# Optimization experiments

Hardware: AMD Instinct MI355X
Metric: run time of the kernel (lower is better)

## Reference

```python
import jax, jax.numpy as jnp
import numpy as np

V = 400000
F = 800000
J = 23
B = 16
PARENTS = np.array([-1, 0, 1, 1, 3, 4, 5, 4, 7, 4, 9, 1, 11, 12, 13, 12, 15, 12, 17, 0, 19, 0, 21])


def setup_inputs() -> dict:
    key = jax.random.key(0)
    ks = jax.random.split(key, 11)
    skin = jax.random.uniform(ks[2], (1, V, J), dtype=jnp.float32)
    skin = skin / skin.sum(-1, keepdims=True)  # convex skinning weights
    return {
        "vertices": jax.random.normal(ks[0], (1, V, 3), jnp.float32),
        "joints": jax.random.normal(ks[1], (1, J, 3), jnp.float32),
        "skinning": skin,
        "joint_0": jax.random.normal(ks[3], (1, 3), jnp.float32),
        "joint_2": jax.random.normal(ks[4], (1, 3), jnp.float32),
        "joint_3": jax.random.normal(ks[5], (1, 3), jnp.float32),
        "joint_4": jax.random.normal(ks[6], (1, 3), jnp.float32),
        "joint_5": jax.random.normal(ks[7], (1, 3), jnp.float32),
        "displacement": jax.random.normal(ks[8], (1, 1, 3), jnp.float32),
        "random_dis": jax.random.normal(ks[9], (3,), jnp.float32),
        "faces": jax.random.randint(ks[10], (F, 3), 0, V, dtype=jnp.int32),
        "batch_size": B,
    }


def rodrigues(aa):
    # aa: [J,3] axis-angle -> [J,3,3] rotation matrices
    angle = jnp.linalg.norm(aa, axis=-1, keepdims=True) + 1e-8  # [J,1]
    axis = aa / angle
    x, y, z = axis[..., 0], axis[..., 1], axis[..., 2]
    zer = jnp.zeros_like(x)
    K = jnp.stack([zer, -z, y, z, zer, -x, -y, x, zer], axis=-1).reshape(aa.shape[0], 3, 3)
    s = jnp.sin(angle)[..., None]
    c = jnp.cos(angle)[..., None]
    eye = jnp.eye(3, dtype=aa.dtype)
    return eye + s * K + (1.0 - c) * (K @ K)


def _forward(vertices, joints, skinning, joint_0, joint_2, joint_3, joint_4, joint_5,
             displacement, random_dis, faces, batch_size):
    dt = vertices.dtype
    half_pi = jnp.asarray(np.pi / 2, dt)
    pose = jnp.zeros((J, 3), dt)
    pose = pose.at[0].set(joint_0[0])
    pose = pose.at[3].set(half_pi * jnp.tanh(joint_2[0]))
    pose = pose.at[11].set(half_pi * jnp.tanh(joint_4[0]))
    pose = pose.at[4].set(half_pi * jnp.tanh(joint_3[0]))
    pose = pose.at[12].set(half_pi * jnp.tanh(joint_5[0]))

    R = rodrigues(pose)                      # [J,3,3]
    j0 = joints[0]                           # [J,3] rest joints
    rel = j0.at[1:].add(-j0[PARENTS[1:]])    # joints relative to parents (root absolute)
    bottom = jnp.tile(jnp.asarray([[[0.0, 0.0, 0.0, 1.0]]], dt), (J, 1, 1))
    mats = jnp.concatenate([jnp.concatenate([R, rel[:, :, None]], axis=2), bottom], axis=1)  # [J,4,4]

    # kinematic-tree scan (J=23, fixed small tree)
    chain = [mats[0]]
    for i in range(1, J):
        chain.append(chain[int(PARENTS[i])] @ mats[i])
    chain = jnp.stack(chain)                 # [J,4,4] global transforms
    posed_joints = chain[:, :3, 3]           # [J,3]

    # relative transforms: remove rest-pose joint contribution
    corr = jnp.einsum('jab,jb->ja', chain[:, :3, :3], j0)
    A = chain.at[:, :3, 3].add(-corr)        # [J,4,4]

    # linear blend skinning
    Tv = jnp.einsum('vj,jab->vab', skinning[0], A)                     # [V,4,4]
    vh = jnp.concatenate([vertices[0], jnp.ones((vertices.shape[1], 1), dt)], axis=1)  # [V,4]
    vp = jnp.einsum('vab,vb->va', Tv, vh)[:, :3]                       # [V,3]

    verts = vp[None] + random_dis[None, None, :] + displacement        # [1,V,3]

    # uniform graph laplacian loss (L = I - D^{-1} A from face edge list)
    f0, f1, f2 = faces[:, 0], faces[:, 1], faces[:, 2]
    ii = jnp.concatenate([f0, f1, f2, f1, f2, f0])
    jj = jnp.concatenate([f1, f2, f0, f0, f1, f2])
    nsum = jax.ops.segment_sum(verts[0][jj], ii, num_segments=V)       # [V,3]
    deg = jax.ops.segment_sum(jnp.ones_like(ii, dtype=dt), ii, num_segments=V)
    Lv = verts[0] - nsum / jnp.maximum(deg, 1.0)[:, None]
    lap = jnp.sum(Lv * Lv)  # batch=1, so mean over batch == sum over (V,3)

    verts_rep = jnp.tile(verts, (batch_size, 1, 1))                    # [B,V,3]
    return verts_rep, lap


def reference(vertices, joints, skinning, joint_0, joint_2, joint_3, joint_4, joint_5,
              displacement, random_dis, faces, batch_size):
    return _forward(vertices, joints, skinning, joint_0, joint_2, joint_3, joint_4, joint_5,
                    displacement, random_dis, faces, batch_size)
```

## Files before the change

kernel.cpp:

```cpp
#include <hip/hip_runtime.h>
#include <math.h>

#define JOINTS 23
#define BATCH 16

#define FPS 128.0f
#define FPS_INV (1.0f / 128.0f)
#define FPB 4096

#define VSHIFT 11
#define VRANGE 2048
#define MAXNB 256
#define NCOPY 64

__global__ void chain_kernel(const float* __restrict__ joints,
                             const float* __restrict__ j0p,
                             const float* __restrict__ j2p,
                             const float* __restrict__ j3p,
                             const float* __restrict__ j4p,
                             const float* __restrict__ j5p,
                             float* __restrict__ Aout,
                             unsigned* __restrict__ gz, int ngz,
                             float* __restrict__ lapz) {
    __shared__ float sJ[JOINTS * 3];
    __shared__ float sM[JOINTS * 12];
    __shared__ float sC[JOINTS * 12];

    const int par[JOINTS]   = {-1,0,1,1,3,4,5,4,7,4,9,1,11,12,13,12,15,12,17,0,19,0,21};
    const int depth[JOINTS] = { 0,1,2,2,3,4,5,4,5,4,5,2, 3, 4, 5, 4, 5, 4, 5,1, 2,1, 2};

    int t = threadIdx.x;
    if (gz) for (int i = t; i < ngz; i += 64) gz[i] = 0u;
    if (lapz && t == 0) *lapz = 0.f;

    for (int i = t; i < JOINTS * 3; i += 64) sJ[i] = joints[i];
    __syncthreads();

    if (t < JOINTS) {
        const float hp = 1.5707963267948966f;
        float px = 0.f, py = 0.f, pz = 0.f;
        if (t == 0)       { px = j0p[0];             py = j0p[1];             pz = j0p[2]; }
        else if (t == 3)  { px = hp * tanhf(j2p[0]); py = hp * tanhf(j2p[1]); pz = hp * tanhf(j2p[2]); }
        else if (t == 4)  { px = hp * tanhf(j3p[0]); py = hp * tanhf(j3p[1]); pz = hp * tanhf(j3p[2]); }
        else if (t == 11) { px = hp * tanhf(j4p[0]); py = hp * tanhf(j4p[1]); pz = hp * tanhf(j4p[2]); }
        else if (t == 12) { px = hp * tanhf(j5p[0]); py = hp * tanhf(j5p[1]); pz = hp * tanhf(j5p[2]); }

        float ang = sqrtf(px * px + py * py + pz * pz) + 1e-8f;
        float ax = px / ang, ay = py / ang, az = pz / ang;
        float s = sinf(ang), c = cosf(ang), oc = 1.f - c;

        float R00 = 1.f + oc * (-(ay * ay + az * az));
        float R01 = -s * az + oc * ax * ay;
        float R02 =  s * ay + oc * ax * az;
        float R10 =  s * az + oc * ax * ay;
        float R11 = 1.f + oc * (-(ax * ax + az * az));
        float R12 = -s * ax + oc * ay * az;
        float R20 = -s * ay + oc * ax * az;
        float R21 =  s * ax + oc * ay * az;
        float R22 = 1.f + oc * (-(ax * ax + ay * ay));

        float rx, ry, rz;
        if (t == 0) { rx = sJ[0]; ry = sJ[1]; rz = sJ[2]; }
        else {
            int p = par[t];
            rx = sJ[t * 3 + 0] - sJ[p * 3 + 0];
            ry = sJ[t * 3 + 1] - sJ[p * 3 + 1];
            rz = sJ[t * 3 + 2] - sJ[p * 3 + 2];
        }
        float* M = &sM[t * 12];
        M[0] = R00; M[1] = R01; M[2]  = R02; M[3]  = rx;
        M[4] = R10; M[5] = R11; M[6]  = R12; M[7]  = ry;
        M[8] = R20; M[9] = R21; M[10] = R22; M[11] = rz;
    }
    __syncthreads();
    if (t == 0) {
        for (int k = 0; k < 12; k++) sC[k] = sM[k];
    }
    __syncthreads();
    for (int d = 1; d <= 5; d++) {
        if (t < JOINTS && depth[t] == d) {
            const float* C = &sC[par[t] * 12];
            const float* M = &sM[t * 12];
            float* D = &sC[t * 12];
            #pragma unroll
            for (int r = 0; r < 3; r++) {
                float c0 = C[r * 4 + 0], c1 = C[r * 4 + 1], c2 = C[r * 4 + 2], c3 = C[r * 4 + 3];
                D[r * 4 + 0] = c0 * M[0] + c1 * M[4] + c2 * M[8];
                D[r * 4 + 1] = c0 * M[1] + c1 * M[5] + c2 * M[9];
                D[r * 4 + 2] = c0 * M[2] + c1 * M[6] + c2 * M[10];
                D[r * 4 + 3] = c0 * M[3] + c1 * M[7] + c2 * M[11] + c3;
            }
        }
        __syncthreads();
    }
    if (t < JOINTS) {
        const float* C = &sC[t * 12];
        float jx = sJ[t * 3 + 0], jy = sJ[t * 3 + 1], jz = sJ[t * 3 + 2];
        #pragma unroll
        for (int r = 0; r < 3; r++) {
            float c0 = C[r * 4 + 0], c1 = C[r * 4 + 1], c2 = C[r * 4 + 2];
            float corr = c0 * jx + c1 * jy + c2 * jz;
            Aout[t * 12 + r * 4 + 0] = c0;
            Aout[t * 12 + r * 4 + 1] = c1;
            Aout[t * 12 + r * 4 + 2] = c2;
            Aout[t * 12 + r * 4 + 3] = C[r * 4 + 3] - corr;
        }
    }
}

__global__ void __launch_bounds__(256) skin_kernel(
        const float* __restrict__ vertices,
        const float* __restrict__ skin,
        const float* __restrict__ A,
        const float* __restrict__ disp,
        const float* __restrict__ rdis,
        float* __restrict__ out,
        int V, int ncopies) {
    __shared__ float sA[JOINTS * 12];
    __shared__ float sS[256 * JOINTS];
    __shared__ float sV[256 * 3];

    int tid = threadIdx.x;
    int v0 = blockIdx.x * 256;
    int nv = V - v0; if (nv > 256) nv = 256;

    for (int i = tid; i < JOINTS * 12; i += 256) sA[i] = A[i];

    int total = nv * JOINTS;
    const float* src = skin + (size_t)v0 * JOINTS;
    int n4 = total >> 2;
    const float4* src4 = (const float4*)src;
    for (int i = tid; i < n4; i += 256) ((float4*)sS)[i] = src4[i];
    for (int i = (n4 << 2) + tid; i < total; i += 256) sS[i] = src[i];
    __syncthreads();

    if (tid < nv) {
        int v = v0 + tid;
        float T[12];
        #pragma unroll
        for (int k = 0; k < 12; k++) T[k] = 0.f;
        #pragma unroll
        for (int j = 0; j < JOINTS; j++) {
            float w = sS[tid * JOINTS + j];
            #pragma unroll
            for (int k = 0; k < 12; k++) T[k] += w * sA[j * 12 + k];
        }
        float x = vertices[v * 3 + 0];
        float y = vertices[v * 3 + 1];
        float z = vertices[v * 3 + 2];
        float a0 = rdis[0] + disp[0];
        float a1 = rdis[1] + disp[1];
        float a2 = rdis[2] + disp[2];
        sV[tid * 3 + 0] = T[0] * x + T[1] * y + T[2]  * z + T[3]  + a0;
        sV[tid * 3 + 1] = T[4] * x + T[5] * y + T[6]  * z + T[7]  + a1;
        sV[tid * 3 + 2] = T[8] * x + T[9] * y + T[10] * z + T[11] + a2;
    }
    __syncthreads();

    int nf = nv * 3;
    int nf4 = nf >> 2;
    for (int b = 0; b < ncopies; b++) {
        float* dst = out + (size_t)b * V * 3 + (size_t)v0 * 3;
        for (int i = tid; i < nf4; i += 256) ((float4*)dst)[i] = ((const float4*)sV)[i];
        for (int i = (nf4 << 2) + tid; i < nf; i += 256) dst[i] = sV[i];
    }
}

__device__ __forceinline__ unsigned long long make_rec(int dest, float sx, float sy, float sz) {
    unsigned qx = (unsigned)(__float2int_rn(sx * FPS) + 8192);
    unsigned qy = (unsigned)(__float2int_rn(sy * FPS) + 8192);
    unsigned qz = (unsigned)(__float2int_rn(sz * FPS) + 8192);
    return (unsigned long long)(unsigned)(dest & (VRANGE - 1))
         | ((unsigned long long)qx << 11)
         | ((unsigned long long)qy << 25)
         | ((unsigned long long)qz << 39);
}

__global__ void __launch_bounds__(1024) build_kernel(
        const int* __restrict__ faces,
        const float* __restrict__ verts,
        unsigned* __restrict__ gcount,
        unsigned long long* __restrict__ recbuf,
        int F, int NB, int CAP) {
    __shared__ unsigned scnt[MAXNB];
    __shared__ unsigned sbase[MAXNB];
    int tid = threadIdx.x;
    for (int i = tid; i < NB; i += 1024) scnt[i] = 0u;
    __syncthreads();

    unsigned long long rec[12];
    unsigned bkt[12];
    unsigned loc[12];
    int valid[4];

    #pragma unroll
    for (int k = 0; k < 4; k++) {
        int f = blockIdx.x * 4096 + k * 1024 + tid;
        valid[k] = (f < F);
        if (valid[k]) {
            int a = __builtin_nontemporal_load(&faces[f * 3 + 0]);
            int b = __builtin_nontemporal_load(&faces[f * 3 + 1]);
            int c = __builtin_nontemporal_load(&faces[f * 3 + 2]);
            float ax = verts[a * 3 + 0], ay = verts[a * 3 + 1], az = verts[a * 3 + 2];
            float bx = verts[b * 3 + 0], by = verts[b * 3 + 1], bz = verts[b * 3 + 2];
            float cx = verts[c * 3 + 0], cy = verts[c * 3 + 1], cz = verts[c * 3 + 2];

            rec[3 * k + 0] = make_rec(a, bx + cx, by + cy, bz + cz);
            rec[3 * k + 1] = make_rec(b, ax + cx, ay + cy, az + cz);
            rec[3 * k + 2] = make_rec(c, ax + bx, ay + by, az + bz);
            unsigned ba = (unsigned)a >> VSHIFT;
            unsigned bb = (unsigned)b >> VSHIFT;
            unsigned bc = (unsigned)c >> VSHIFT;
            bkt[3 * k + 0] = ba; loc[3 * k + 0] = atomicAdd(&scnt[ba], 1u);
            bkt[3 * k + 1] = bb; loc[3 * k + 1] = atomicAdd(&scnt[bb], 1u);
            bkt[3 * k + 2] = bc; loc[3 * k + 2] = atomicAdd(&scnt[bc], 1u);
        }
    }
    __syncthreads();

    if (tid < NB) {
        int b = tid + (int)(blockIdx.x % (unsigned)NB);
        if (b >= NB) b -= NB;
        unsigned n = scnt[b];
        sbase[b] = n ? atomicAdd(&gcount[b], n) : 0u;
    }
    __syncthreads();

    #pragma unroll
    for (int k = 0; k < 4; k++) {
        if (valid[k]) {
            #pragma unroll
            for (int j = 0; j < 3; j++) {
                unsigned bb = bkt[3 * k + j];
                unsigned idx = sbase[bb] + loc[3 * k + j];
                if (idx < (unsigned)CAP)
                    recbuf[(size_t)bb * CAP + idx] = rec[3 * k + j];
            }
        }
    }
}

__global__ void __launch_bounds__(1024) reduce_kernel(
        const float* __restrict__ verts,
        const unsigned* __restrict__ gcount,
        const unsigned long long* __restrict__ recbuf,
        float* __restrict__ out,
        float* __restrict__ lap,
        int V, int NB, int CAP) {
    __shared__ unsigned long long lacc[VRANGE];
    __shared__ float partial[16];
    int tid = threadIdx.x;
    int blk = blockIdx.x;

    if (blk >= NB) {
        int cb = blk - NB;
        size_t nf = (size_t)V * 3;
        size_t nf4 = nf >> 2;
        const float4* src4 = (const float4*)out;
        for (int b = 1; b < BATCH; b++) {
            float4* dst4 = (float4*)(out + (size_t)b * nf);
            for (size_t i = (size_t)cb * 1024 + tid; i < nf4; i += (size_t)NCOPY * 1024)
                dst4[i] = src4[i];
        }
        size_t rem = nf & 3;
        if (cb == 0 && (size_t)tid < rem) {
            size_t base = nf4 << 2;
            for (int b = 1; b < BATCH; b++)
                out[(size_t)b * nf + base + tid] = out[base + tid];
        }
        return;
    }

    lacc[tid] = 0ull;
    lacc[tid + 1024] = 0ull;
    __syncthreads();

    int cnt = (int)gcount[blk];
    if (cnt > CAP) cnt = CAP;
    const unsigned long long* buf = recbuf + (size_t)blk * CAP;
    for (int i = tid; i < cnt; i += 1024) {
        unsigned long long r = buf[i];
        unsigned d  = (unsigned)r & (VRANGE - 1);
        unsigned qx = ((unsigned)(r >> 11)) & 0x3FFFu;
        unsigned qy = ((unsigned)(r >> 25)) & 0x3FFFu;
        unsigned qz = ((unsigned)(r >> 39)) & 0x3FFFu;
        unsigned long long add = (unsigned long long)(qx - 4096u)
            | ((unsigned long long)(qy - 4096u) << 20)
            | ((unsigned long long)(qz - 4096u) << 40)
            | (1ull << 59);
        atomicAdd(&lacc[d], add);
    }
    __syncthreads();

    float e = 0.f;
    int v0 = blk << VSHIFT;
    #pragma unroll
    for (int k = 0; k < 2; k++) {
        int v = v0 + k * 1024 + tid;
        if (v < V) {
            unsigned long long u = lacc[k * 1024 + tid];
            long long c2 = (long long)(u >> 59);
            long long zs = (long long)((u >> 40) & 0x7FFFFull);
            long long ys = (long long)((u >> 20) & 0xFFFFFull);
            long long xs = (long long)(u & 0xFFFFFull);
            float vx = verts[v * 3 + 0];
            float vy = verts[v * 3 + 1];
            float vz = verts[v * 3 + 2];
            float lx, ly, lz;
            if (c2 == 0) {
                lx = vx; ly = vy; lz = vz;
            } else {
                float inv = 1.f / (2.f * (float)c2);
                float nx = (float)(xs - c2 * FPB) * FPS_INV;
                float ny = (float)(ys - c2 * FPB) * FPS_INV;
                float nz = (float)(zs - c2 * FPB) * FPS_INV;
                lx = vx - nx * inv;
                ly = vy - ny * inv;
                lz = vz - nz * inv;
            }
            e += lx * lx + ly * ly + lz * lz;
        }
    }
    #pragma unroll
    for (int off = 32; off > 0; off >>= 1) e += __shfl_down(e, off, 64);
    int lane = tid & 63;
    int wid = tid >> 6;
    if (lane == 0) partial[wid] = e;
    __syncthreads();
    if (tid == 0) {
        float s = 0.f;
        #pragma unroll
        for (int w = 0; w < 16; w++) s += partial[w];
        atomicAdd(lap, s);
    }
}

__device__ __forceinline__ unsigned long long pack_corner(float sx, float sy, float sz) {
    unsigned long long ex = (unsigned)(__float2int_rn(sx * FPS) + FPB);
    unsigned long long ey = (unsigned)(__float2int_rn(sy * FPS) + FPB);
    unsigned long long ez = (unsigned)(__float2int_rn(sz * FPS) + FPB);
    return ex | (ey << 20) | (ez << 40) | (1ull << 59);
}

__global__ void __launch_bounds__(256) scatter_dev_kernel(
        const int* __restrict__ faces,
        const float* __restrict__ verts,
        unsigned long long* __restrict__ acc,
        int F) {
    int f = blockIdx.x * blockDim.x + threadIdx.x;
    if (f >= F) return;
    int a = __builtin_nontemporal_load(&faces[f * 3 + 0]);
    int b = __builtin_nontemporal_load(&faces[f * 3 + 1]);
    int c = __builtin_nontemporal_load(&faces[f * 3 + 2]);
    float ax = verts[a * 3 + 0], ay = verts[a * 3 + 1], az = verts[a * 3 + 2];
    float bx = verts[b * 3 + 0], by = verts[b * 3 + 1], bz = verts[b * 3 + 2];
    float cx = verts[c * 3 + 0], cy = verts[c * 3 + 1], cz = verts[c * 3 + 2];
    atomicAdd(&acc[a], pack_corner(bx + cx, by + cy, bz + cz));
    atomicAdd(&acc[b], pack_corner(ax + cx, ay + cy, az + cz));
    atomicAdd(&acc[c], pack_corner(ax + bx, ay + by, az + bz));
}

__global__ void __launch_bounds__(256) lap_reduce_kernel(
        const float* __restrict__ verts,
        const unsigned long long* __restrict__ acc,
        float* __restrict__ lap,
        int V) {
    int v = blockIdx.x * blockDim.x + threadIdx.x;
    float e = 0.f;
    if (v < V) {
        unsigned long long u = acc[v];
        long long cnt = (long long)(u >> 59);
        long long zs  = (long long)((u >> 40) & 0x7FFFFull);
        long long ys  = (long long)((u >> 20) & 0xFFFFFull);
        long long xs  = (long long)(u & 0xFFFFFull);
        float vx = verts[v * 3 + 0];
        float vy = verts[v * 3 + 1];
        float vz = verts[v * 3 + 2];
        float lx, ly, lz;
        if (cnt == 0) {
            lx = vx; ly = vy; lz = vz;
        } else {
            float inv = 1.f / (2.f * (float)cnt);
            float nx = (float)(xs - cnt * FPB) * FPS_INV;
            float ny = (float)(ys - cnt * FPB) * FPS_INV;
            float nz = (float)(zs - cnt * FPB) * FPS_INV;
            lx = vx - nx * inv;
            ly = vy - ny * inv;
            lz = vz - nz * inv;
        }
        e = lx * lx + ly * ly + lz * lz;
    }
    #pragma unroll
    for (int off = 32; off > 0; off >>= 1) e += __shfl_down(e, off, 64);
    __shared__ float partial[4];
    int lane = threadIdx.x & 63;
    int wid = threadIdx.x >> 6;
    if (lane == 0) partial[wid] = e;
    __syncthreads();
    if (threadIdx.x == 0) {
        float s = partial[0] + partial[1] + partial[2] + partial[3];
        atomicAdd(lap, s);
    }
}

__global__ void scatter_kernel(const int* __restrict__ faces,
                               const float* __restrict__ verts,
                               float* __restrict__ nsum,
                               float* __restrict__ deg,
                               int F) {
    int f = blockIdx.x * blockDim.x + threadIdx.x;
    if (f >= F) return;
    int a = faces[f * 3 + 0];
    int b = faces[f * 3 + 1];
    int c = faces[f * 3 + 2];
    float ax = verts[a * 3 + 0], ay = verts[a * 3 + 1], az = verts[a * 3 + 2];
    float bx = verts[b * 3 + 0], by = verts[b * 3 + 1], bz = verts[b * 3 + 2];
    float cx = verts[c * 3 + 0], cy = verts[c * 3 + 1], cz = verts[c * 3 + 2];
    atomicAdd(&nsum[a * 3 + 0], bx + cx);
    atomicAdd(&nsum[a * 3 + 1], by + cy);
    atomicAdd(&nsum[a * 3 + 2], bz + cz);
    atomicAdd(&nsum[b * 3 + 0], ax + cx);
    atomicAdd(&nsum[b * 3 + 1], ay + cy);
    atomicAdd(&nsum[b * 3 + 2], az + cz);
    atomicAdd(&nsum[c * 3 + 0], ax + bx);
    atomicAdd(&nsum[c * 3 + 1], ay + by);
    atomicAdd(&nsum[c * 3 + 2], az + bz);
    atomicAdd(&deg[a], 2.f);
    atomicAdd(&deg[b], 2.f);
    atomicAdd(&deg[c], 2.f);
}

__global__ void lap_kernel(const float* __restrict__ verts,
                           const float* __restrict__ nsum,
                           const float* __restrict__ deg,
                           float* __restrict__ lap,
                           int V) {
    int v = blockIdx.x * blockDim.x + threadIdx.x;
    float acc = 0.f;
    if (v < V) {
        float d = deg[v];
        if (d < 1.f) d = 1.f;
        float inv = 1.f / d;
        float lx = verts[v * 3 + 0] - nsum[v * 3 + 0] * inv;
        float ly = verts[v * 3 + 1] - nsum[v * 3 + 1] * inv;
        float lz = verts[v * 3 + 2] - nsum[v * 3 + 2] * inv;
        acc = lx * lx + ly * ly + lz * lz;
    }
    #pragma unroll
    for (int off = 32; off > 0; off >>= 1) acc += __shfl_down(acc, off, 64);
    __shared__ float partial[4];
    int lane = threadIdx.x & 63;
    int wid = threadIdx.x >> 6;
    if (lane == 0) partial[wid] = acc;
    __syncthreads();
    if (threadIdx.x == 0) {
        float s = partial[0] + partial[1] + partial[2] + partial[3];
        atomicAdd(lap, s);
    }
}

extern "C" void kernel_launch(void* const* d_in, const int* in_sizes, int n_in,
                              void* d_out, int out_size, void* d_ws, size_t ws_size,
                              hipStream_t stream) {
    const float* vertices = (const float*)d_in[0];
    const float* joints   = (const float*)d_in[1];
    const float* skin     = (const float*)d_in[2];
    const float* j0p      = (const float*)d_in[3];
    const float* j2p      = (const float*)d_in[4];
    const float* j3p      = (const float*)d_in[5];
    const float* j4p      = (const float*)d_in[6];
    const float* j5p      = (const float*)d_in[7];
    const float* disp     = (const float*)d_in[8];
    const float* rdis     = (const float*)d_in[9];
    const int*   faces    = (const int*)d_in[10];
    float* out = (float*)d_out;

    int V = in_sizes[0] / 3;
    int F = in_sizes[10] / 3;

    char* ws = (char*)d_ws;
    float* A = (float*)ws;
    float* lap = out + (size_t)BATCH * V * 3;

    int NB = (V + VRANGE - 1) >> VSHIFT;
    long avg = (NB > 0) ? (3L * F) / NB : 0;
    long capL = avg + avg / 8 + 1024;
    int CAP = (int)((capL + 255) & ~255L);
    size_t recOff = 4096 + 1024;
    size_t needFast = recOff + (size_t)NB * (size_t)CAP * 8;
    bool fastOK = (V <= (1 << 19)) && NB >= 1 && NB <= MAXNB && (ws_size >= needFast);
    size_t needMid = 4096 + (size_t)V * 8;

    int nb256 = (V + 255) / 256;

    if (fastOK) {
        unsigned* gcount = (unsigned*)(ws + 4096);
        unsigned long long* recbuf = (unsigned long long*)(ws + recOff);
        chain_kernel<<<1, 64, 0, stream>>>(joints, j0p, j2p, j3p, j4p, j5p, A,
                                           gcount, NB, lap);
        skin_kernel<<<nb256, 256, 0, stream>>>(vertices, skin, A, disp, rdis, out, V, 1);
        int b1 = (F + 4095) / 4096;
        build_kernel<<<b1, 1024, 0, stream>>>(faces, out, gcount, recbuf, F, NB, CAP);
        reduce_kernel<<<NB + NCOPY, 1024, 0, stream>>>(out, gcount, recbuf, out, lap, V, NB, CAP);
    } else if (ws_size >= needMid) {
        unsigned long long* acc = (unsigned long long*)(ws + 4096);
        chain_kernel<<<1, 64, 0, stream>>>(joints, j0p, j2p, j3p, j4p, j5p, A,
                                           (unsigned*)nullptr, 0, lap);
        hipMemsetAsync(acc, 0, (size_t)V * 8, stream);
        skin_kernel<<<nb256, 256, 0, stream>>>(vertices, skin, A, disp, rdis, out, V, BATCH);
        scatter_dev_kernel<<<(F + 255) / 256, 256, 0, stream>>>(faces, out, acc, F);
        lap_reduce_kernel<<<nb256, 256, 0, stream>>>(out, acc, lap, V);
    } else {
        float* nsum = (float*)(ws + 4096);
        float* deg  = (float*)(ws + 4096 + (size_t)V * 3 * 4);
        chain_kernel<<<1, 64, 0, stream>>>(joints, j0p, j2p, j3p, j4p, j5p, A,
                                           (unsigned*)nullptr, 0, lap);
        hipMemsetAsync(nsum, 0, (size_t)V * 16, stream);
        skin_kernel<<<nb256, 256, 0, stream>>>(vertices, skin, A, disp, rdis, out, V, BATCH);
        scatter_kernel<<<(F + 255) / 256, 256, 0, stream>>>(faces, out, nsum, deg, F);
        lap_kernel<<<nb256, 256, 0, stream>>>(out, nsum, deg, lap, V);
    }
}
```

Before: 200.9 us.

## Replicate batch copies via dynamic work-stealing across all reduce blocks

```diff
diff --git a/kernel.cpp b/kernel.cpp
--- a/kernel.cpp
+++ b/kernel.cpp
@@ -11,7 +11,10 @@
 #define VSHIFT 11
 #define VRANGE 2048
 #define MAXNB 256
-#define NCOPY 64
+#define RTOT 512
+#define CH_REG 2048
+
+typedef float f4 __attribute__((ext_vector_type(4)));
 
 __global__ void chain_kernel(const float* __restrict__ joints,
                              const float* __restrict__ j0p,
@@ -234,7 +237,8 @@
                 unsigned bb = bkt[3 * k + j];
                 unsigned idx = sbase[bb] + loc[3 * k + j];
                 if (idx < (unsigned)CAP)
-                    recbuf[(size_t)bb * CAP + idx] = rec[3 * k + j];
+                    __builtin_nontemporal_store(rec[3 * k + j],
+                                                &recbuf[(size_t)bb * CAP + idx]);
             }
         }
     }
@@ -246,92 +250,115 @@
         const unsigned long long* __restrict__ recbuf,
         float* __restrict__ out,
         float* __restrict__ lap,
+        unsigned* __restrict__ gwork,
         int V, int NB, int CAP) {
     __shared__ unsigned long long lacc[VRANGE];
     __shared__ float partial[16];
+    __shared__ unsigned swork;
     int tid = threadIdx.x;
     int blk = blockIdx.x;
 
-    if (blk >= NB) {
-        int cb = blk - NB;
-        size_t nf = (size_t)V * 3;
-        size_t nf4 = nf >> 2;
-        const float4* src4 = (const float4*)out;
-        for (int b = 1; b < BATCH; b++) {
-            float4* dst4 = (float4*)(out + (size_t)b * nf);
-            for (size_t i = (size_t)cb * 1024 + tid; i < nf4; i += (size_t)NCOPY * 1024)
-                dst4[i] = src4[i];
-        }
-        size_t rem = nf & 3;
-        if (cb == 0 && (size_t)tid < rem) {
-            size_t base = nf4 << 2;
+    if (blk < NB) {
+        lacc[tid] = 0ull;
+        lacc[tid + 1024] = 0ull;
+        __syncthreads();
+
+        int cnt = (int)gcount[blk];
+        if (cnt > CAP) cnt = CAP;
+        const unsigned long long* buf = recbuf + (size_t)blk * CAP;
+        for (int i = tid; i < cnt; i += 1024) {
+            unsigned long long r = __builtin_nontemporal_load(&buf[i]);
+            unsigned d  = (unsigned)r & (VRANGE - 1);
+            unsigned qx = ((unsigned)(r >> 11)) & 0x3FFFu;
+            unsigned qy = ((unsigned)(r >> 25)) & 0x3FFFu;
+            unsigned qz = ((unsigned)(r >> 39)) & 0x3FFFu;
+            unsigned long long add = (unsigned long long)(qx - 4096u)
+                | ((unsigned long long)(qy - 4096u) << 20)
+                | ((unsigned long long)(qz - 4096u) << 40)
+                | (1ull << 59);
+            atomicAdd(&lacc[d], add);
+        }
+        __syncthreads();
+
+        float e = 0.f;
+        int v0 = blk << VSHIFT;
+        #pragma unroll
+        for (int k = 0; k < 2; k++) {
+            int v = v0 + k * 1024 + tid;
+            if (v < V) {
+                unsigned long long u = lacc[k * 1024 + tid];
+                long long c2 = (long long)(u >> 59);
+                long long zs = (long long)((u >> 40) & 0x7FFFFull);
+                long long ys = (long long)((u >> 20) & 0xFFFFFull);
+                long long xs = (long long)(u & 0xFFFFFull);
+                float vx = verts[v * 3 + 0];
+                float vy = verts[v * 3 + 1];
+                float vz = verts[v * 3 + 2];
+                float lx, ly, lz;
+                if (c2 == 0) {
+                    lx = vx; ly = vy; lz = vz;
+                } else {
+                    float inv = 1.f / (2.f * (float)c2);
+                    float nx = (float)(xs - c2 * FPB) * FPS_INV;
+                    float ny = (float)(ys - c2 * FPB) * FPS_INV;
+                    float nz = (float)(zs - c2 * FPB) * FPS_INV;
+                    lx = vx - nx * inv;
+                    ly = vy - ny * inv;
+                    lz = vz - nz * inv;
+                }
+                e += lx * lx + ly * ly + lz * lz;
+            }
+        }
+        #pragma unroll
+        for (int off = 32; off > 0; off >>= 1) e += __shfl_down(e, off, 64);
+        int lane = tid & 63;
+        int wid = tid >> 6;
+        if (lane == 0) partial[wid] = e;
+        __syncthreads();
+        if (tid == 0) {
+            float s = 0.f;
+            #pragma unroll
+            for (int w = 0; w < 16; w++) s += partial[w];
+            atomicAdd(lap, s);
+        }
+    }
+
+    unsigned nf = (unsigned)(V * 3);
+    unsigned nf4 = nf >> 2;
+
+    if (blk == NB) {
+        unsigned rem = nf & 3u;
+        if ((unsigned)tid < rem) {
+            size_t base = (size_t)nf4 * 4 + tid;
             for (int b = 1; b < BATCH; b++)
-                out[(size_t)b * nf + base + tid] = out[base + tid];
-        }
-        return;
-    }
-
-    lacc[tid] = 0ull;
-    lacc[tid + 1024] = 0ull;
-    __syncthreads();
-
-    int cnt = (int)gcount[blk];
-    if (cnt > CAP) cnt = CAP;
-    const unsigned long long* buf = recbuf + (size_t)blk * CAP;
-    for (int i = tid; i < cnt; i += 1024) {
-        unsigned long long r = buf[i];
-        unsigned d  = (unsigned)r & (VRANGE - 1);
-        unsigned qx = ((unsigned)(r >> 11)) & 0x3FFFu;
-        unsigned qy = ((unsigned)(r >> 25)) & 0x3FFFu;
-        unsigned qz = ((unsigned)(r >> 39)) & 0x3FFFu;
-        unsigned long long add = (unsigned long long)(qx - 4096u)
-            | ((unsigned long long)(qy - 4096u) << 20)
-            | ((unsigned long long)(qz - 4096u) << 40)
-            | (1ull << 59);
-        atomicAdd(&lacc[d], add);
-    }
-    __syncthreads();
-
-    float e = 0.f;
-    int v0 = blk << VSHIFT;
-    #pragma unroll
-    for (int k = 0; k < 2; k++) {
-        int v = v0 + k * 1024 + tid;
-        if (v < V) {
-            unsigned long long u = lacc[k * 1024 + tid];
-            long long c2 = (long long)(u >> 59);
-            long long zs = (long long)((u >> 40) & 0x7FFFFull);
-            long long ys = (long long)((u >> 20) & 0xFFFFFull);
-            long long xs = (long long)(u & 0xFFFFFull);
-            float vx = verts[v * 3 + 0];
-            float vy = verts[v * 3 + 1];
-            float vz = verts[v * 3 + 2];
-            float lx, ly, lz;
-            if (c2 == 0) {
-                lx = vx; ly = vy; lz = vz;
-            } else {
-                float inv = 1.f / (2.f * (float)c2);
-                float nx = (float)(xs - c2 * FPB) * FPS_INV;
-                float ny = (float)(ys - c2 * FPB) * FPS_INV;
-                float nz = (float)(zs - c2 * FPB) * FPS_INV;
-                lx = vx - nx * inv;
-                ly = vy - ny * inv;
-                lz = vz - nz * inv;
+                out[(size_t)b * nf + base] = out[base];
+        }
+    }
+
+    unsigned ncpb = (nf4 + (CH_REG - 1)) / CH_REG;
+    unsigned total = 3u * ncpb;
+    const f4* src4 = (const f4*)out;
+    for (;;) {
+        __syncthreads();
+        if (tid == 0) swork = atomicAdd(gwork, 1u);
+        __syncthreads();
+        unsigned w = swork;
+        if (w >= total) break;
+        unsigned g = w / ncpb;
+        unsigned r = w - g * ncpb;
+        size_t i0 = (size_t)r * CH_REG;
+        #pragma unroll
+        for (int j = 0; j < CH_REG / 1024; j++) {
+            size_t idx = i0 + (size_t)j * 1024 + tid;
+            if (idx < nf4) {
+                f4 v = src4[idx];
+                #pragma unroll
+                for (int k = 0; k < 5; k++) {
+                    int b = 1 + (int)g * 5 + k;
+                    __builtin_nontemporal_store(v, (f4*)(out + (size_t)b * nf) + idx);
+                }
             }
-            e += lx * lx + ly * ly + lz * lz;
-        }
-    }
-    #pragma unroll
-    for (int off = 32; off > 0; off >>= 1) e += __shfl_down(e, off, 64);
-    int lane = tid & 63;
-    int wid = tid >> 6;
-    if (lane == 0) partial[wid] = e;
-    __syncthreads();
-    if (tid == 0) {
-        float s = 0.f;
-        #pragma unroll
-        for (int w = 0; w < 16; w++) s += partial[w];
-        atomicAdd(lap, s);
+        }
     }
 }
 
@@ -486,22 +513,25 @@
     long avg = (NB > 0) ? (3L * F) / NB : 0;
     long capL = avg + avg / 8 + 1024;
     int CAP = (int)((capL + 255) & ~255L);
-    size_t recOff = 4096 + 1024;
+    size_t recOff = 4096 + 1088;
     size_t needFast = recOff + (size_t)NB * (size_t)CAP * 8;
-    bool fastOK = (V <= (1 << 19)) && NB >= 1 && NB <= MAXNB && (ws_size >= needFast);
+    bool fastOK = (V <= (1 << 19)) && NB >= 1 && NB <= MAXNB && (ws_size >= needFast)
+                  && (BATCH == 16);
     size_t needMid = 4096 + (size_t)V * 8;
 
     int nb256 = (V + 255) / 256;
 
     if (fastOK) {
         unsigned* gcount = (unsigned*)(ws + 4096);
+        unsigned* gwork  = gcount + 256;
         unsigned long long* recbuf = (unsigned long long*)(ws + recOff);
         chain_kernel<<<1, 64, 0, stream>>>(joints, j0p, j2p, j3p, j4p, j5p, A,
-                                           gcount, NB, lap);
+                                           gcount, 257, lap);
         skin_kernel<<<nb256, 256, 0, stream>>>(vertices, skin, A, disp, rdis, out, V, 1);
         int b1 = (F + 4095) / 4096;
         build_kernel<<<b1, 1024, 0, stream>>>(faces, out, gcount, recbuf, F, NB, CAP);
-        reduce_kernel<<<NB + NCOPY, 1024, 0, stream>>>(out, gcount, recbuf, out, lap, V, NB, CAP);
+        reduce_kernel<<<RTOT, 1024, 0, stream>>>(out, gcount, recbuf, out, lap,
+                                                 gwork, V, NB, CAP);
     } else if (ws_size >= needMid) {
         unsigned long long* acc = (unsigned long long*)(ws + 4096);
         chain_kernel<<<1, 64, 0, stream>>>(joints, j0p, j2p, j3p, j4p, j5p, A,
```

Result: slower. 269.7 us (+34.2%).
